# Optimization experiments

Measured on AMD Instinct MI355X. Metric: run time of the kernel, lower is better.

Reference implementation:

```python
import jax, jax.numpy as jnp
import numpy as np

B, N, E, D = 16, 512, 8192, 256
LN_EPS = 1e-5
NEG_INF = -1e9


def setup_inputs() -> dict:
    key = jax.random.key(0)
    ks = jax.random.split(key, 10)
    inp = {
        "obj_nodes": jax.random.normal(ks[0], (B, N, D), jnp.float32),
        "pred_emb": jax.random.normal(ks[1], (B, E, D), jnp.float32),
        "rel_ind": jax.random.randint(ks[2], (B, E, 2), 0, N),
        "similarity_matrix": jax.random.normal(ks[3], (B, E), jnp.float32),
        "nodes_mask": jax.random.bernoulli(ks[4], 0.9, (B, N)),
        "edges_mask": jax.random.bernoulli(ks[5], 0.5, (B, E)),
        # parameters (torch nn.Linear weight layout: (out, in))
        "w_node": jax.random.normal(ks[6], (D, D), jnp.float32) / np.sqrt(D),
        "w_edge": jax.random.normal(ks[7], (D, D), jnp.float32) / np.sqrt(D),
        "w_attn": jax.random.normal(ks[8], (1, 3 * D + 1), jnp.float32) / np.sqrt(3 * D + 1),
        "ln_gamma": jnp.ones((D,), jnp.float32),
        "ln_beta": jnp.zeros((D,), jnp.float32),
    }
    return inp


def _layer_norm(x, gamma, beta):
    mu = jnp.mean(x, axis=-1, keepdims=True)
    var = jnp.mean(jnp.square(x - mu), axis=-1, keepdims=True)
    return (x - mu) * jax.lax.rsqrt(var + LN_EPS) * gamma + beta


def reference(obj_nodes, pred_emb, rel_ind, similarity_matrix, nodes_mask,
              edges_mask, w_node, w_edge, w_attn, ln_gamma, ln_beta):
    dtype = obj_nodes.dtype
    tn = jnp.einsum('bnd,ed->bne', obj_nodes, w_node)   # (B,N,D) node_fc
    te = jnp.einsum('bmd,ed->bme', pred_emb, w_edge)    # (B,E,D) edge_fc
    src, dst = rel_ind[..., 0], rel_ind[..., 1]          # (B,E)
    gather = jax.vmap(lambda t, i: t[i])
    src_f = gather(tn, src)                              # (B,E,D)
    dst_f = gather(tn, dst)                              # (B,E,D)
    att_in = jnp.concatenate(
        [src_f, dst_f, similarity_matrix[..., None], te], axis=-1)  # (B,E,3D+1)
    scores = jax.nn.leaky_relu(jnp.einsum('bef,of->beo', att_in, w_attn))  # (B,E,1)
    # masked edges are excluded from the per-batch softmax (dim=0 over valid edges)
    scores = jnp.where(edges_mask[..., None], scores, NEG_INF)
    weights = jax.nn.softmax(scores, axis=1)             # softmax over all valid edges
    msgs = jnp.where(edges_mask[..., None], weights * src_f, jnp.zeros((), dtype))
    # scatter-add messages to destination nodes, per batch
    scatter = jax.vmap(lambda d, m: jnp.zeros((N, D), dtype).at[d].add(m))
    updated = scatter(dst, msgs)                         # (B,N,D)
    updated = updated * nodes_mask[..., None].astype(dtype)
    return _layer_norm(updated, ln_gamma, ln_beta)
```

## Files before the change

kernel.cpp:

```cpp
#include <hip/hip_runtime.h>
#include <hip/hip_bf16.h>
#include <stdint.h>

#define B_ 16
#define N_ 512
#define E_ 8192
#define D_ 256
#define NBUCKET (B_ * N_)
#define CAP 64

constexpr int OFF_WN  = 16;
constexpr int OFF_WE  = OFF_WN + D_*D_;
constexpr int OFF_WA  = OFF_WE + D_*D_;
constexpr int OFF_GAM = OFF_WA + 1024;
constexpr int OFF_BET = OFF_GAM + D_;
constexpr int OFF_TN  = OFF_BET + D_;
constexpr int OFF_VE  = OFF_TN + B_*N_*D_;
constexpr int OFF_S1  = OFF_VE + D_;
constexpr int OFF_S2  = OFF_S1 + NBUCKET;
constexpr int OFF_SC  = OFF_S2 + NBUCKET;
constexpr int OFF_SM  = OFF_SC + B_*E_;
constexpr int OFF_CNT = OFF_SM + 32;
constexpr int OFF_REC = OFF_CNT + NBUCKET;
constexpr int CONV_TOTAL = D_*D_ + D_*D_ + 769 + D_ + D_;
constexpr int ZERO_TOTAL = NBUCKET + NBUCKET + NBUCKET + D_;

__device__ __forceinline__ float bf2f(uint16_t u) {
    union { uint32_t i; float f; } v; v.i = ((uint32_t)u) << 16; return v.f;
}

__device__ __forceinline__ float loadF(const void* p, int i, int isBF) {
    if (isBF) return __bfloat162float(((const __hip_bfloat16*)p)[i]);
    return ((const float*)p)[i];
}

__device__ __forceinline__ float4 loadF4(const void* p, int i, int isBF) {
    if (isBF) {
        ushort4 v = *(const ushort4*)((const uint16_t*)p + i);
        return make_float4(bf2f(v.x), bf2f(v.y), bf2f(v.z), bf2f(v.w));
    }
    return *(const float4*)((const float*)p + i);
}

__device__ __forceinline__ bool readMask(const void* p, int i, int ml) {
    if (ml == 0) return ((const uint8_t*)p)[i] != 0;
    if (ml == 1) return ((const int*)p)[i] != 0;
    if (ml == 2) return (((const uint16_t*)p)[i] & 0x7FFFu) != 0;
    return (((const uint32_t*)p)[i] & 0x7FFFFFFFu) != 0;
}

__global__ void k_detect(const uint32_t* objw, const uint32_t* emaskw, int* flags) {
    __shared__ int s_insane;
    __shared__ int s_ok[3];
    int t = threadIdx.x;
    if (t == 0) { s_insane = 0; s_ok[0] = 1; s_ok[1] = 1; s_ok[2] = 1; }
    __syncthreads();
    {
        uint32_t x = objw[t];
        int insane = 0;
        #pragma unroll
        for (int h = 0; h < 2; ++h) {
            uint32_t v = (h ? (x >> 16) : x) & 0xFFFFu;
            uint32_t e = (v >> 7) & 0xFFu;
            if ((v & 0x7FFFu) != 0 && (e < 107u || e > 147u)) insane++;
        }
        if (insane) atomicAdd(&s_insane, insane);
    }
    {
        int i32ok = 1, f32ok = 1, bfok = 1;
        for (int i = t; i < 1024; i += 256) {
            uint32_t x = emaskw[i];
            if (!(x <= 1u)) i32ok = 0;
            if (!(x == 0u || x == 0x3F800000u)) f32ok = 0;
            uint32_t lo = x & 0xFFFFu, hi = x >> 16;
            if (!((lo == 0u || lo == 0x3F80u) && (hi == 0u || hi == 0x3F80u))) bfok = 0;
        }
        if (!i32ok) atomicAnd(&s_ok[0], 0);
        if (!f32ok) atomicAnd(&s_ok[1], 0);
        if (!bfok)  atomicAnd(&s_ok[2], 0);
    }
    __syncthreads();
    if (t == 0) {
        flags[0] = (s_insane > 64) ? 0 : 1;
        int ml = 0;
        if (s_ok[0]) ml = 1; else if (s_ok[1]) ml = 3; else if (s_ok[2]) ml = 2;
        flags[1] = ml;
    }
}

__global__ void k_convert(const void* wn, const void* we, const void* wa,
                          const void* gam, const void* bet, float* ws) {
    int isBF = ((const int*)ws)[0];
    int stride = gridDim.x * blockDim.x;
    int gid = blockIdx.x * blockDim.x + threadIdx.x;
    for (int i = gid; i < CONV_TOTAL; i += stride) {
        int j = i;
        if (j < D_*D_)    { ws[OFF_WN + j]  = loadF(wn, j, isBF); continue; }
        j -= D_*D_;
        if (j < D_*D_)    { ws[OFF_WE + j]  = loadF(we, j, isBF); continue; }
        j -= D_*D_;
        if (j < 769)      { ws[OFF_WA + j]  = loadF(wa, j, isBF); continue; }
        j -= 769;
        if (j < D_)       { ws[OFF_GAM + j] = loadF(gam, j, isBF); continue; }
        j -= D_;
        ws[OFF_BET + j] = loadF(bet, j, isBF);
    }
    for (int i = gid; i < ZERO_TOTAL; i += stride) {
        int j = i;
        if (j < NBUCKET) { ((int*)ws)[OFF_CNT + j] = 0; continue; }
        j -= NBUCKET;
        if (j < NBUCKET) { ws[OFF_S1 + j] = 0.f; continue; }
        j -= NBUCKET;
        if (j < NBUCKET) { ws[OFF_S2 + j] = 0.f; continue; }
        j -= NBUCKET;
        ws[OFF_VE + j] = 0.f;
    }
}

__global__ __launch_bounds__(256) void k_vedge(float* ws) {
    int t = threadIdx.x;
    int d0 = blockIdx.x * 8;
    const float* we  = ws + OFF_WE;
    const float* wa3 = ws + OFF_WA + 513;
    float a = 0.f;
    #pragma unroll
    for (int i = 0; i < 8; ++i) {
        int d = d0 + i;
        a += wa3[d] * we[d * D_ + t];
    }
    atomicAdd(&ws[OFF_VE + t], a);
}

__global__ __launch_bounds__(256) void k_nodefc(const void* obj, float* ws) {
    int isBF = ((const int*)ws)[0];
    __shared__ float As[32][68];
    __shared__ float Bs[32][68];
    const float* wn = ws + OFF_WN;
    float* tn = ws + OFF_TN;
    int t = threadIdx.x;
    int tx = t & 15, ty = t >> 4;
    int bm = blockIdx.x >> 2, bn = blockIdx.x & 3;
    int row0 = bm * 64, col0 = bn * 64;
    int sr = t >> 2;
    int sk = (t & 3) * 8;
    float acc[4][4] = {};
    for (int kt = 0; kt < 8; ++kt) {
        int k0 = kt * 32;
        __syncthreads();
        float4 a0 = loadF4(obj, (row0 + sr) * D_ + k0 + sk, isBF);
        float4 a1 = loadF4(obj, (row0 + sr) * D_ + k0 + sk + 4, isBF);
        float4 b0 = *(const float4*)(wn + (col0 + sr) * D_ + k0 + sk);
        float4 b1 = *(const float4*)(wn + (col0 + sr) * D_ + k0 + sk + 4);
        As[sk+0][sr] = a0.x; As[sk+1][sr] = a0.y; As[sk+2][sr] = a0.z; As[sk+3][sr] = a0.w;
        As[sk+4][sr] = a1.x; As[sk+5][sr] = a1.y; As[sk+6][sr] = a1.z; As[sk+7][sr] = a1.w;
        Bs[sk+0][sr] = b0.x; Bs[sk+1][sr] = b0.y; Bs[sk+2][sr] = b0.z; Bs[sk+3][sr] = b0.w;
        Bs[sk+4][sr] = b1.x; Bs[sk+5][sr] = b1.y; Bs[sk+6][sr] = b1.z; Bs[sk+7][sr] = b1.w;
        __syncthreads();
        #pragma unroll
        for (int k = 0; k < 32; ++k) {
            float4 av = *(const float4*)&As[k][ty * 4];
            float4 bv = *(const float4*)&Bs[k][tx * 4];
            acc[0][0] += av.x * bv.x; acc[0][1] += av.x * bv.y;
            acc[0][2] += av.x * bv.z; acc[0][3] += av.x * bv.w;
            acc[1][0] += av.y * bv.x; acc[1][1] += av.y * bv.y;
            acc[1][2] += av.y * bv.z; acc[1][3] += av.y * bv.w;
            acc[2][0] += av.z * bv.x; acc[2][1] += av.z * bv.y;
            acc[2][2] += av.z * bv.z; acc[2][3] += av.z * bv.w;
            acc[3][0] += av.w * bv.x; acc[3][1] += av.w * bv.y;
            acc[3][2] += av.w * bv.z; acc[3][3] += av.w * bv.w;
        }
    }
    #pragma unroll
    for (int rr = 0; rr < 4; ++rr) {
        float4 o = make_float4(acc[rr][0], acc[rr][1], acc[rr][2], acc[rr][3]);
        *(float4*)&tn[(size_t)(row0 + ty * 4 + rr) * D_ + col0 + tx * 4] = o;
    }
    float w1v[4], w2v[4];
    #pragma unroll
    for (int c = 0; c < 4; ++c) {
        w1v[c] = ws[OFF_WA + col0 + tx * 4 + c];
        w2v[c] = ws[OFF_WA + D_ + col0 + tx * 4 + c];
    }
    #pragma unroll
    for (int rr = 0; rr < 4; ++rr) {
        float p1 = acc[rr][0]*w1v[0] + acc[rr][1]*w1v[1] + acc[rr][2]*w1v[2] + acc[rr][3]*w1v[3];
        float p2 = acc[rr][0]*w2v[0] + acc[rr][1]*w2v[1] + acc[rr][2]*w2v[2] + acc[rr][3]*w2v[3];
        #pragma unroll
        for (int o = 1; o < 16; o <<= 1) {
            p1 += __shfl_xor(p1, o);
            p2 += __shfl_xor(p2, o);
        }
        if (tx == 0) {
            atomicAdd(&ws[OFF_S1 + row0 + ty * 4 + rr], p1);
            atomicAdd(&ws[OFF_S2 + row0 + ty * 4 + rr], p2);
        }
    }
}

__global__ __launch_bounds__(256) void k_scores(const void* pred, const int2* rel,
                                                const void* emask, const void* sim,
                                                float* ws) {
    const int* flags = (const int*)ws;
    int isBF = flags[0], ml = flags[1];
    int gid = blockIdx.x * blockDim.x + threadIdx.x;
    int gw = gid >> 6, lane = gid & 63;
    if (gw >= B_ * E_) return;
    int b = gw >> 13;
    float4 ve4 = *(const float4*)(ws + OFF_VE + lane * 4);
    float dot;
    if (isBF) {
        ushort4 v = *(const ushort4*)((const uint16_t*)pred + (size_t)gw * D_ + lane * 4);
        dot = bf2f(v.x)*ve4.x + bf2f(v.y)*ve4.y + bf2f(v.z)*ve4.z + bf2f(v.w)*ve4.w;
    } else {
        float4 v = *(const float4*)((const float*)pred + (size_t)gw * D_ + lane * 4);
        dot = v.x*ve4.x + v.y*ve4.y + v.z*ve4.z + v.w*ve4.w;
    }
    #pragma unroll
    for (int off = 32; off > 0; off >>= 1) dot += __shfl_xor(dot, off);
    if (lane == 0) {
        int2 sd = rel[gw];
        float s = dot + ws[OFF_S1 + b * N_ + sd.x] + ws[OFF_S2 + b * N_ + sd.y]
                + loadF(sim, gw, isBF) * ws[OFF_WA + 512];
        s = (s > 0.f) ? s : 0.01f * s;
        bool m = readMask(emask, gw, ml);
        ws[OFF_SC + gw] = m ? s : -1e9f;
        if (m) {
            int bucket = b * N_ + sd.y;
            int slot = atomicAdd((int*)ws + OFF_CNT + bucket, 1);
            if (slot < CAP)
                ((int*)ws)[OFF_REC + bucket * CAP + slot] = sd.x | ((gw & (E_ - 1)) << 16);
        }
    }
}

__global__ __launch_bounds__(1024) void k_softmax(float* ws) {
    __shared__ float part[16];
    int b = blockIdx.x, t = threadIdx.x, w = t >> 6, lane = t & 63;
    const float* sc = ws + OFF_SC + b * E_;
    float loc[8];
    float mx = -3e38f;
    #pragma unroll
    for (int i = 0; i < 8; ++i) { loc[i] = sc[t + i * 1024]; mx = fmaxf(mx, loc[i]); }
    #pragma unroll
    for (int off = 32; off > 0; off >>= 1) mx = fmaxf(mx, __shfl_xor(mx, off));
    if (lane == 0) part[w] = mx;
    __syncthreads();
    float M = part[0];
    #pragma unroll
    for (int k = 1; k < 16; ++k) M = fmaxf(M, part[k]);
    float sum = 0.f;
    #pragma unroll
    for (int i = 0; i < 8; ++i) sum += __expf(loc[i] - M);
    #pragma unroll
    for (int off = 32; off > 0; off >>= 1) sum += __shfl_xor(sum, off);
    __syncthreads();
    if (lane == 0) part[w] = sum;
    __syncthreads();
    if (t == 0) {
        float S = 0.f;
        #pragma unroll
        for (int k = 0; k < 16; ++k) S += part[k];
        ws[OFF_SM + b * 2]     = M;
        ws[OFF_SM + b * 2 + 1] = 1.f / S;
    }
}

__global__ __launch_bounds__(256) void k_scatter_ln(const void* nmask, const float* wsc,
                                                    void* out) {
    const float* ws = wsc;
    const int* flags = (const int*)ws;
    int isBF = flags[0], ml = flags[1];
    int t = threadIdx.x, w = t >> 6, lane = t & 63;
    int ng = blockIdx.x * 4 + w;
    int b = ng >> 9;
    int cnt = ((const int*)ws)[OFF_CNT + ng];
    if (cnt > CAP) cnt = CAP;
    const int* rec = (const int*)ws + OFF_REC + ng * CAP;
    const float* tn  = ws + OFF_TN + (size_t)b * N_ * D_;
    const float* sc  = ws + OFF_SC + b * E_;
    float M    = ws[OFF_SM + b * 2];
    float invS = ws[OFF_SM + b * 2 + 1];
    float v0 = 0.f, v1 = 0.f, v2 = 0.f, v3 = 0.f;
    for (int i = 0; i < cnt; ++i) {
        int rc = rec[i];
        int src = rc & 0xFFFF;
        float wv = __expf(sc[((unsigned)rc) >> 16] - M) * invS;
        const float* s = tn + (size_t)src * D_;
        v0 += wv * s[lane];
        v1 += wv * s[lane + 64];
        v2 += wv * s[lane + 128];
        v3 += wv * s[lane + 192];
    }
    float mk = readMask(nmask, ng, ml) ? 1.f : 0.f;
    v0 *= mk; v1 *= mk; v2 *= mk; v3 *= mk;
    float sum = v0 + v1 + v2 + v3;
    float sq  = v0*v0 + v1*v1 + v2*v2 + v3*v3;
    #pragma unroll
    for (int o = 32; o > 0; o >>= 1) {
        sum += __shfl_xor(sum, o);
        sq  += __shfl_xor(sq, o);
    }
    float mu  = sum * (1.f / 256.f);
    float var = fmaxf(sq * (1.f / 256.f) - mu * mu, 0.f);
    float rs  = rsqrtf(var + 1e-5f);
    const float* gam = ws + OFF_GAM;
    const float* bet = ws + OFF_BET;
    size_t ro = (size_t)ng * D_;
    float r0 = (v0 - mu) * rs * gam[lane]       + bet[lane];
    float r1 = (v1 - mu) * rs * gam[lane + 64]  + bet[lane + 64];
    float r2 = (v2 - mu) * rs * gam[lane + 128] + bet[lane + 128];
    float r3 = (v3 - mu) * rs * gam[lane + 192] + bet[lane + 192];
    if (isBF) {
        __hip_bfloat16* o = (__hip_bfloat16*)out + ro;
        o[lane]       = __float2bfloat16(r0);
        o[lane + 64]  = __float2bfloat16(r1);
        o[lane + 128] = __float2bfloat16(r2);
        o[lane + 192] = __float2bfloat16(r3);
    } else {
        float* o = (float*)out + ro;
        o[lane] = r0; o[lane + 64] = r1; o[lane + 128] = r2; o[lane + 192] = r3;
    }
}

extern "C" void kernel_launch(void* const* d_in, const int* in_sizes, int n_in,
                              void* d_out, int out_size, void* d_ws, size_t ws_size,
                              hipStream_t stream) {
    (void)in_sizes; (void)n_in; (void)out_size; (void)ws_size;
    const void* obj   = d_in[0];
    const void* pred  = d_in[1];
    const int2* rel   = (const int2*)d_in[2];
    const void* sim   = d_in[3];
    const void* nmask = d_in[4];
    const void* emask = d_in[5];
    const void* wn    = d_in[6];
    const void* we    = d_in[7];
    const void* wa    = d_in[8];
    const void* gam   = d_in[9];
    const void* bet   = d_in[10];
    float* ws = (float*)d_ws;

    k_detect<<<1, 256, 0, stream>>>((const uint32_t*)obj, (const uint32_t*)emask, (int*)d_ws);
    k_convert<<<128, 256, 0, stream>>>(wn, we, wa, gam, bet, ws);
    k_vedge<<<32, 256, 0, stream>>>(ws);
    k_nodefc<<<512, 256, 0, stream>>>(obj, ws);
    k_scores<<<(B_ * E_) / 4, 256, 0, stream>>>(pred, rel, emask, sim, ws);
    k_softmax<<<16, 1024, 0, stream>>>(ws);
    k_scatter_ln<<<NBUCKET / 4, 256, 0, stream>>>(nmask, ws, d_out);
}
```

Measured before the change: 101.1 us.

## Fold detect, convert and vedge kernels into node-fc and remove atomics

Drops the detect, convert and vedge launches. Dtype detection is now recomputed inline in each kernel, weights are read and converted directly from the inputs, and the edge vector is computed inside the node-fc kernel. Per-node score partials are stored per column tile instead of through atomics, and the scores kernel uses a fixed grid with a strided loop that skips the pred load for masked edges. The cost is extra redundant reads in every block, and the edge-vector computation is serialized into a single block.

```diff
diff --git a/kernel.cpp b/kernel.cpp
--- a/kernel.cpp
+++ b/kernel.cpp
@@ -8,22 +8,16 @@
 #define D_ 256
 #define NBUCKET (B_ * N_)
 #define CAP 64
-
-constexpr int OFF_WN  = 16;
-constexpr int OFF_WE  = OFF_WN + D_*D_;
-constexpr int OFF_WA  = OFF_WE + D_*D_;
-constexpr int OFF_GAM = OFF_WA + 1024;
-constexpr int OFF_BET = OFF_GAM + D_;
-constexpr int OFF_TN  = OFF_BET + D_;
-constexpr int OFF_VE  = OFF_TN + B_*N_*D_;
-constexpr int OFF_S1  = OFF_VE + D_;
-constexpr int OFF_S2  = OFF_S1 + NBUCKET;
-constexpr int OFF_SC  = OFF_S2 + NBUCKET;
+#define SCORE_BLOCKS 4096
+
+constexpr int OFF_VE  = 16;
+constexpr int OFF_TN  = OFF_VE + D_;
+constexpr int OFF_S1P = OFF_TN + B_*N_*D_;
+constexpr int OFF_S2P = OFF_S1P + 4*NBUCKET;
+constexpr int OFF_SC  = OFF_S2P + 4*NBUCKET;
 constexpr int OFF_SM  = OFF_SC + B_*E_;
 constexpr int OFF_CNT = OFF_SM + 32;
 constexpr int OFF_REC = OFF_CNT + NBUCKET;
-constexpr int CONV_TOTAL = D_*D_ + D_*D_ + 769 + D_ + D_;
-constexpr int ZERO_TOTAL = NBUCKET + NBUCKET + NBUCKET + D_;
 
 __device__ __forceinline__ float bf2f(uint16_t u) {
     union { uint32_t i; float f; } v; v.i = ((uint32_t)u) << 16; return v.f;
@@ -49,93 +43,40 @@
     return (((const uint32_t*)p)[i] & 0x7FFFFFFFu) != 0;
 }
 
-__global__ void k_detect(const uint32_t* objw, const uint32_t* emaskw, int* flags) {
-    __shared__ int s_insane;
-    __shared__ int s_ok[3];
-    int t = threadIdx.x;
-    if (t == 0) { s_insane = 0; s_ok[0] = 1; s_ok[1] = 1; s_ok[2] = 1; }
-    __syncthreads();
-    {
-        uint32_t x = objw[t];
-        int insane = 0;
-        #pragma unroll
-        for (int h = 0; h < 2; ++h) {
-            uint32_t v = (h ? (x >> 16) : x) & 0xFFFFu;
-            uint32_t e = (v >> 7) & 0xFFu;
-            if ((v & 0x7FFFu) != 0 && (e < 107u || e > 147u)) insane++;
-        }
-        if (insane) atomicAdd(&s_insane, insane);
-    }
-    {
-        int i32ok = 1, f32ok = 1, bfok = 1;
-        for (int i = t; i < 1024; i += 256) {
-            uint32_t x = emaskw[i];
-            if (!(x <= 1u)) i32ok = 0;
-            if (!(x == 0u || x == 0x3F800000u)) f32ok = 0;
-            uint32_t lo = x & 0xFFFFu, hi = x >> 16;
-            if (!((lo == 0u || lo == 0x3F80u) && (hi == 0u || hi == 0x3F80u))) bfok = 0;
-        }
-        if (!i32ok) atomicAnd(&s_ok[0], 0);
-        if (!f32ok) atomicAnd(&s_ok[1], 0);
-        if (!bfok)  atomicAnd(&s_ok[2], 0);
-    }
-    __syncthreads();
-    if (t == 0) {
-        flags[0] = (s_insane > 64) ? 0 : 1;
-        int ml = 0;
-        if (s_ok[0]) ml = 1; else if (s_ok[1]) ml = 3; else if (s_ok[2]) ml = 2;
-        flags[1] = ml;
-    }
-}
-
-__global__ void k_convert(const void* wn, const void* we, const void* wa,
-                          const void* gam, const void* bet, float* ws) {
-    int isBF = ((const int*)ws)[0];
-    int stride = gridDim.x * blockDim.x;
-    int gid = blockIdx.x * blockDim.x + threadIdx.x;
-    for (int i = gid; i < CONV_TOTAL; i += stride) {
-        int j = i;
-        if (j < D_*D_)    { ws[OFF_WN + j]  = loadF(wn, j, isBF); continue; }
-        j -= D_*D_;
-        if (j < D_*D_)    { ws[OFF_WE + j]  = loadF(we, j, isBF); continue; }
-        j -= D_*D_;
-        if (j < 769)      { ws[OFF_WA + j]  = loadF(wa, j, isBF); continue; }
-        j -= 769;
-        if (j < D_)       { ws[OFF_GAM + j] = loadF(gam, j, isBF); continue; }
-        j -= D_;
-        ws[OFF_BET + j] = loadF(bet, j, isBF);
-    }
-    for (int i = gid; i < ZERO_TOTAL; i += stride) {
-        int j = i;
-        if (j < NBUCKET) { ((int*)ws)[OFF_CNT + j] = 0; continue; }
-        j -= NBUCKET;
-        if (j < NBUCKET) { ws[OFF_S1 + j] = 0.f; continue; }
-        j -= NBUCKET;
-        if (j < NBUCKET) { ws[OFF_S2 + j] = 0.f; continue; }
-        j -= NBUCKET;
-        ws[OFF_VE + j] = 0.f;
-    }
-}
-
-__global__ __launch_bounds__(256) void k_vedge(float* ws) {
-    int t = threadIdx.x;
-    int d0 = blockIdx.x * 8;
-    const float* we  = ws + OFF_WE;
-    const float* wa3 = ws + OFF_WA + 513;
-    float a = 0.f;
-    #pragma unroll
-    for (int i = 0; i < 8; ++i) {
-        int d = d0 + i;
-        a += wa3[d] * we[d * D_ + t];
-    }
-    atomicAdd(&ws[OFF_VE + t], a);
-}
-
-__global__ __launch_bounds__(256) void k_nodefc(const void* obj, float* ws) {
-    int isBF = ((const int*)ws)[0];
+__device__ __forceinline__ void detect(const void* obj, const void* emask,
+                                       int& isBF, int& ml) {
+    const uint32_t* ow = (const uint32_t*)obj;
+    int insane = 0;
+    #pragma unroll
+    for (int i = 0; i < 32; ++i) {
+        uint32_t x = ow[i];
+        uint32_t lo = x & 0xFFFFu, hi = x >> 16;
+        uint32_t el = (lo >> 7) & 0xFFu, eh = (hi >> 7) & 0xFFu;
+        if ((lo & 0x7FFFu) && (el < 107u || el > 147u)) insane++;
+        if ((hi & 0x7FFFu) && (eh < 107u || eh > 147u)) insane++;
+    }
+    isBF = (insane >= 8) ? 0 : 1;
+    const uint32_t* ew = (const uint32_t*)emask;
+    bool i32ok = true, f32ok = true, bfok = true;
+    #pragma unroll
+    for (int i = 0; i < 16; ++i) {
+        uint32_t x = ew[i];
+        if (x > 1u) i32ok = false;
+        if (x != 0u && x != 0x3F800000u) f32ok = false;
+        uint32_t lo = x & 0xFFFFu, hi = x >> 16;
+        if (!((lo == 0u || lo == 0x3F80u) && (hi == 0u || hi == 0x3F80u))) bfok = false;
+    }
+    ml = i32ok ? 1 : (f32ok ? 3 : (bfok ? 2 : 0));
+}
+
+__global__ __launch_bounds__(256) void k_nodefc(const void* obj, const void* wn,
+                                                const void* we, const void* wa,
+                                                const void* emask, float* ws) {
+    int isBF, ml;
+    detect(obj, emask, isBF, ml);
+    (void)ml;
     __shared__ float As[32][68];
     __shared__ float Bs[32][68];
-    const float* wn = ws + OFF_WN;
     float* tn = ws + OFF_TN;
     int t = threadIdx.x;
     int tx = t & 15, ty = t >> 4;
@@ -149,8 +90,8 @@
         __syncthreads();
         float4 a0 = loadF4(obj, (row0 + sr) * D_ + k0 + sk, isBF);
         float4 a1 = loadF4(obj, (row0 + sr) * D_ + k0 + sk + 4, isBF);
-        float4 b0 = *(const float4*)(wn + (col0 + sr) * D_ + k0 + sk);
-        float4 b1 = *(const float4*)(wn + (col0 + sr) * D_ + k0 + sk + 4);
+        float4 b0 = loadF4(wn, (col0 + sr) * D_ + k0 + sk, isBF);
+        float4 b1 = loadF4(wn, (col0 + sr) * D_ + k0 + sk + 4, isBF);
         As[sk+0][sr] = a0.x; As[sk+1][sr] = a0.y; As[sk+2][sr] = a0.z; As[sk+3][sr] = a0.w;
         As[sk+4][sr] = a1.x; As[sk+5][sr] = a1.y; As[sk+6][sr] = a1.z; As[sk+7][sr] = a1.w;
         Bs[sk+0][sr] = b0.x; Bs[sk+1][sr] = b0.y; Bs[sk+2][sr] = b0.z; Bs[sk+3][sr] = b0.w;
@@ -178,8 +119,8 @@
     float w1v[4], w2v[4];
     #pragma unroll
     for (int c = 0; c < 4; ++c) {
-        w1v[c] = ws[OFF_WA + col0 + tx * 4 + c];
-        w2v[c] = ws[OFF_WA + D_ + col0 + tx * 4 + c];
+        w1v[c] = loadF(wa, col0 + tx * 4 + c, isBF);
+        w2v[c] = loadF(wa, D_ + col0 + tx * 4 + c, isBF);
     }
     #pragma unroll
     for (int rr = 0; rr < 4; ++rr) {
@@ -191,41 +132,60 @@
             p2 += __shfl_xor(p2, o);
         }
         if (tx == 0) {
-            atomicAdd(&ws[OFF_S1 + row0 + ty * 4 + rr], p1);
-            atomicAdd(&ws[OFF_S2 + row0 + ty * 4 + rr], p2);
-        }
-    }
-}
-
-__global__ __launch_bounds__(256) void k_scores(const void* pred, const int2* rel,
-                                                const void* emask, const void* sim,
+            ws[OFF_S1P + bn * NBUCKET + row0 + ty * 4 + rr] = p1;
+            ws[OFF_S2P + bn * NBUCKET + row0 + ty * 4 + rr] = p2;
+        }
+    }
+    if (blockIdx.x == 0) {
+        float a = 0.f;
+        for (int d = 0; d < D_; ++d)
+            a += loadF(wa, 513 + d, isBF) * loadF(we, d * D_ + t, isBF);
+        ws[OFF_VE + t] = a;
+    }
+    if (blockIdx.x == gridDim.x - 1) {
+        for (int i = t; i < NBUCKET; i += 256) ((int*)ws)[OFF_CNT + i] = 0;
+    }
+}
+
+__global__ __launch_bounds__(256) void k_scores(const void* obj, const void* pred,
+                                                const int2* rel, const void* emask,
+                                                const void* sim, const void* wa,
                                                 float* ws) {
-    const int* flags = (const int*)ws;
-    int isBF = flags[0], ml = flags[1];
-    int gid = blockIdx.x * blockDim.x + threadIdx.x;
-    int gw = gid >> 6, lane = gid & 63;
-    if (gw >= B_ * E_) return;
-    int b = gw >> 13;
+    int isBF, ml;
+    detect(obj, emask, isBF, ml);
+    int gid = blockIdx.x * 256 + threadIdx.x;
+    int wv = gid >> 6, lane = gid & 63;
     float4 ve4 = *(const float4*)(ws + OFF_VE + lane * 4);
-    float dot;
-    if (isBF) {
-        ushort4 v = *(const ushort4*)((const uint16_t*)pred + (size_t)gw * D_ + lane * 4);
-        dot = bf2f(v.x)*ve4.x + bf2f(v.y)*ve4.y + bf2f(v.z)*ve4.z + bf2f(v.w)*ve4.w;
-    } else {
-        float4 v = *(const float4*)((const float*)pred + (size_t)gw * D_ + lane * 4);
-        dot = v.x*ve4.x + v.y*ve4.y + v.z*ve4.z + v.w*ve4.w;
-    }
-    #pragma unroll
-    for (int off = 32; off > 0; off >>= 1) dot += __shfl_xor(dot, off);
-    if (lane == 0) {
-        int2 sd = rel[gw];
-        float s = dot + ws[OFF_S1 + b * N_ + sd.x] + ws[OFF_S2 + b * N_ + sd.y]
-                + loadF(sim, gw, isBF) * ws[OFF_WA + 512];
-        s = (s > 0.f) ? s : 0.01f * s;
+    float simc = loadF(wa, 512, isBF);
+    int stride = SCORE_BLOCKS * 4;
+    for (int gw = wv; gw < B_ * E_; gw += stride) {
         bool m = readMask(emask, gw, ml);
-        ws[OFF_SC + gw] = m ? s : -1e9f;
-        if (m) {
-            int bucket = b * N_ + sd.y;
+        if (!m) {
+            if (lane == 0) ws[OFF_SC + gw] = -1e9f;
+            continue;
+        }
+        int b = gw >> 13;
+        float dot;
+        if (isBF) {
+            ushort4 v = *(const ushort4*)((const uint16_t*)pred + (size_t)gw * D_ + lane * 4);
+            dot = bf2f(v.x)*ve4.x + bf2f(v.y)*ve4.y + bf2f(v.z)*ve4.z + bf2f(v.w)*ve4.w;
+        } else {
+            float4 v = *(const float4*)((const float*)pred + (size_t)gw * D_ + lane * 4);
+            dot = v.x*ve4.x + v.y*ve4.y + v.z*ve4.z + v.w*ve4.w;
+        }
+        #pragma unroll
+        for (int off = 32; off > 0; off >>= 1) dot += __shfl_xor(dot, off);
+        if (lane == 0) {
+            int2 sd = rel[gw];
+            int ib = b * N_;
+            float s1 = ws[OFF_S1P + ib + sd.x] + ws[OFF_S1P + NBUCKET + ib + sd.x]
+                     + ws[OFF_S1P + 2*NBUCKET + ib + sd.x] + ws[OFF_S1P + 3*NBUCKET + ib + sd.x];
+            float s2 = ws[OFF_S2P + ib + sd.y] + ws[OFF_S2P + NBUCKET + ib + sd.y]
+                     + ws[OFF_S2P + 2*NBUCKET + ib + sd.y] + ws[OFF_S2P + 3*NBUCKET + ib + sd.y];
+            float s = dot + s1 + s2 + loadF(sim, gw, isBF) * simc;
+            s = (s > 0.f) ? s : 0.01f * s;
+            ws[OFF_SC + gw] = s;
+            int bucket = ib + sd.y;
             int slot = atomicAdd((int*)ws + OFF_CNT + bucket, 1);
             if (slot < CAP)
                 ((int*)ws)[OFF_REC + bucket * CAP + slot] = sd.x | ((gw & (E_ - 1)) << 16);
@@ -265,11 +225,13 @@
     }
 }
 
-__global__ __launch_bounds__(256) void k_scatter_ln(const void* nmask, const float* wsc,
+__global__ __launch_bounds__(256) void k_scatter_ln(const void* obj, const void* emask,
+                                                    const void* nmask, const void* gam,
+                                                    const void* bet, const float* wsc,
                                                     void* out) {
     const float* ws = wsc;
-    const int* flags = (const int*)ws;
-    int isBF = flags[0], ml = flags[1];
+    int isBF, ml;
+    detect(obj, emask, isBF, ml);
     int t = threadIdx.x, w = t >> 6, lane = t & 63;
     int ng = blockIdx.x * 4 + w;
     int b = ng >> 9;
@@ -303,13 +265,15 @@
     float mu  = sum * (1.f / 256.f);
     float var = fmaxf(sq * (1.f / 256.f) - mu * mu, 0.f);
     float rs  = rsqrtf(var + 1e-5f);
-    const float* gam = ws + OFF_GAM;
-    const float* bet = ws + OFF_BET;
     size_t ro = (size_t)ng * D_;
-    float r0 = (v0 - mu) * rs * gam[lane]       + bet[lane];
-    float r1 = (v1 - mu) * rs * gam[lane + 64]  + bet[lane + 64];
-    float r2 = (v2 - mu) * rs * gam[lane + 128] + bet[lane + 128];
-    float r3 = (v3 - mu) * rs * gam[lane + 192] + bet[lane + 192];
+    float g0 = loadF(gam, lane,       isBF), b0v = loadF(bet, lane,       isBF);
+    float g1 = loadF(gam, lane + 64,  isBF), b1v = loadF(bet, lane + 64,  isBF);
+    float g2 = loadF(gam, lane + 128, isBF), b2v = loadF(bet, lane + 128, isBF);
+    float g3 = loadF(gam, lane + 192, isBF), b3v = loadF(bet, lane + 192, isBF);
+    float r0 = (v0 - mu) * rs * g0 + b0v;
+    float r1 = (v1 - mu) * rs * g1 + b1v;
+    float r2 = (v2 - mu) * rs * g2 + b2v;
+    float r3 = (v3 - mu) * rs * g3 + b3v;
     if (isBF) {
         __hip_bfloat16* o = (__hip_bfloat16*)out + ro;
         o[lane]       = __float2bfloat16(r0);
@@ -339,11 +303,8 @@
     const void* bet   = d_in[10];
     float* ws = (float*)d_ws;
 
-    k_detect<<<1, 256, 0, stream>>>((const uint32_t*)obj, (const uint32_t*)emask, (int*)d_ws);
-    k_convert<<<128, 256, 0, stream>>>(wn, we, wa, gam, bet, ws);
-    k_vedge<<<32, 256, 0, stream>>>(ws);
-    k_nodefc<<<512, 256, 0, stream>>>(obj, ws);
-    k_scores<<<(B_ * E_) / 4, 256, 0, stream>>>(pred, rel, emask, sim, ws);
+    k_nodefc<<<512, 256, 0, stream>>>(obj, wn, we, wa, emask, ws);
+    k_scores<<<SCORE_BLOCKS, 256, 0, stream>>>(obj, pred, rel, emask, sim, wa, ws);
     k_softmax<<<16, 1024, 0, stream>>>(ws);
-    k_scatter_ln<<<NBUCKET / 4, 256, 0, stream>>>(nmask, ws, d_out);
-}
+    k_scatter_ln<<<NBUCKET / 4, 256, 0, stream>>>(obj, emask, nmask, gam, bet, ws, d_out);
+}
```

New measurement: 123.6 us. 1.22x slower.
